# Kernel tuning notes

Measured on AMD Instinct MI355X. Metric: run time of the kernel, lower is better.

## Reference

```python
import jax, jax.numpy as jnp
import numpy as np

# dims (must match init_kwargs / input_specs)
B_SZ = 1024
STOCH = 1024
ACT = 32
DETER = 4096
TOKENS = 8
TOKEN_DIM = DETER // TOKENS          # 512
EXPAND = 2
HIDDEN = EXPAND * TOKEN_DIM          # 1024
NHEADS = 8
HEADDIM = HIDDEN // NHEADS           # 128
DSTATE = 64
K = 4                                # conv kernel
LAYERS = 2
CONV_DIM = HIDDEN + 2 * DSTATE       # 1152
IN_PROJ_DIM = HIDDEN + CONV_DIM + NHEADS
EPS = 1e-4


def rmsnorm(x, w):
    return x * jax.lax.rsqrt(jnp.mean(x * x, axis=-1, keepdims=True) + EPS) * w


def silu(x):
    return x * jax.nn.sigmoid(x)


def setup_inputs() -> dict:
    key = jax.random.key(0)
    ks = jax.random.split(key, 16)

    def lin(k, shape, fan_in):
        return jax.random.normal(k, shape, jnp.float32) / np.sqrt(fan_in)

    # dt_bias init (inverse softplus of log-uniform dt in [1e-3, 1e-1])
    u = jax.random.uniform(ks[0], (LAYERS, NHEADS))
    dt = jnp.exp(u * (np.log(0.1) - np.log(0.001)) + np.log(0.001))
    dt = jnp.maximum(dt, 1e-4)
    dt_bias = dt + jnp.log(-jnp.expm1(-dt))

    return {
        "stoch": jax.random.normal(ks[1], (B_SZ, STOCH), jnp.float32),
        "deter": jax.random.normal(ks[2], (B_SZ, DETER), jnp.float32),
        "action": jax.random.normal(ks[3], (B_SZ, ACT), jnp.float32),
        "conv_state": jax.random.normal(ks[4], (LAYERS, B_SZ, CONV_DIM, K - 1), jnp.float32),
        "ssm_state": jax.random.normal(ks[5], (LAYERS, B_SZ, NHEADS, HEADDIM, DSTATE), jnp.float32),
        # input_proj: Linear(stoch+act -> token_dim) + RMSNorm + SiLU
        "in_proj_w": lin(ks[6], (TOKEN_DIM, STOCH + ACT), STOCH + ACT),
        "in_proj_b": jnp.zeros((TOKEN_DIM,), jnp.float32),
        "in_norm_w": jnp.ones((TOKEN_DIM,), jnp.float32),
        # per-block params, stacked over layers
        "blk_norm_w": jnp.ones((LAYERS, TOKEN_DIM), jnp.float32),
        "blk_in_w": lin(ks[7], (LAYERS, IN_PROJ_DIM, TOKEN_DIM), TOKEN_DIM),
        "blk_conv_w": lin(ks[8], (LAYERS, CONV_DIM, K), K),
        "blk_conv_b": jnp.zeros((LAYERS, CONV_DIM), jnp.float32),
        "blk_A_log": jnp.log(jax.random.uniform(ks[9], (LAYERS, NHEADS), minval=1.0, maxval=16.0)),
        "blk_D": jnp.ones((LAYERS, NHEADS), jnp.float32),
        "blk_dt_bias": dt_bias.astype(jnp.float32),
        "blk_post_norm_w": jnp.ones((LAYERS, HIDDEN), jnp.float32),
        "blk_out_w": lin(ks[10], (LAYERS, TOKEN_DIM, HIDDEN), HIDDEN),
        "blk_out_b": jnp.zeros((LAYERS, TOKEN_DIM), jnp.float32),
        "out_norm_w": jnp.ones((TOKEN_DIM,), jnp.float32),
    }


def reference(stoch, deter, action, conv_state, ssm_state,
              in_proj_w, in_proj_b, in_norm_w,
              blk_norm_w, blk_in_w, blk_conv_w, blk_conv_b,
              blk_A_log, blk_D, blk_dt_bias, blk_post_norm_w,
              blk_out_w, blk_out_b, out_norm_w):
    b = action.shape[0]
    # action normalization with detached denominator
    action = action / jax.lax.stop_gradient(jnp.maximum(jnp.abs(action), 1.0))
    inp = jnp.concatenate([stoch.reshape(b, -1), action], axis=-1)
    tok = silu(rmsnorm(inp @ in_proj_w.T + in_proj_b, in_norm_w))  # (B, token_dim)

    def block_step(x, layer):
        nw, iw, cw, cb, alog, dskip, dtb, pw, ow, ob, cs, ss = layer
        h = rmsnorm(x, nw)
        proj = h @ iw.T  # (B, hidden + conv_dim + nheads)
        z = proj[:, :HIDDEN]
        xBC = proj[:, HIDDEN:HIDDEN + CONV_DIM]
        dt_raw = proj[:, HIDDEN + CONV_DIM:]
        # depthwise causal conv on xBC with persistent state
        seq = jnp.concatenate([cs, xBC[:, :, None]], axis=-1)  # (B, conv_dim, K)
        conv = silu(jnp.einsum('ck,bck->bc', cw, seq) + cb)
        new_cs = seq[:, :, 1:]
        x_post = conv[:, :HIDDEN]
        Bp = conv[:, HIDDEN:HIDDEN + DSTATE]
        Cp = conv[:, HIDDEN + DSTATE:]
        xh = x_post.reshape(b, NHEADS, HEADDIM)
        # SSD single-step recurrence
        dt = jax.nn.softplus(dt_raw + dtb)           # (B, H)
        dA = jnp.exp(dt * (-jnp.exp(alog)))          # (B, H)
        dBx = jnp.einsum('bh,bn,bhp->bhpn', dt, Bp, xh)
        new_ss = ss * dA[:, :, None, None] + dBx     # (B, H, P, N)
        y = jnp.einsum('bhpn,bn->bhp', new_ss, Cp) + dskip[None, :, None] * xh
        gated = rmsnorm(y.reshape(b, HIDDEN) * silu(z), pw)
        out = gated @ ow.T + ob
        return x + out, (new_cs, new_ss)

    layers = (blk_norm_w, blk_in_w, blk_conv_w, blk_conv_b, blk_A_log, blk_D,
              blk_dt_bias, blk_post_norm_w, blk_out_w, blk_out_b,
              conv_state, ssm_state)
    x_final, (new_conv_state, new_ssm_state) = jax.lax.scan(block_step, tok, layers)

    x_t = rmsnorm(x_final, out_norm_w)  # (B, token_dim)
    # rolling tape of last TOKENS final-block outputs
    tape = deter.reshape(b, TOKENS, TOKEN_DIM)
    new_deter = jnp.concatenate([tape[:, 1:], x_t[:, None, :]], axis=1).reshape(b, DETER)
    return (new_deter, new_conv_state, new_ssm_state)
```

## Files before the change

### kernel.cpp

```cpp
#include <hip/hip_runtime.h>
#include <hip/hip_bf16.h>
#include <math.h>

#define B_SZ 1024
#define STOCH 1024
#define ACT 32
#define DETER 4096
#define TOKEN_DIM 512
#define HIDDEN 1024
#define NHEADS 8
#define HEADDIM 128
#define DSTATE 64
#define CONV_DIM 1152
#define IN_PROJ_DIM 2184
#define IPP2 2304
#define KIN 1088
#define EPS 0.0001f

typedef float f32x4 __attribute__((ext_vector_type(4)));
typedef __bf16 bf16x8 __attribute__((ext_vector_type(8)));
typedef __bf16 bf16x4 __attribute__((ext_vector_type(4)));

#define N0C (512 * KIN / 4)
#define N1C (2 * IPP2 * TOKEN_DIM / 4)
#define N2C (2 * TOKEN_DIM * HIDDEN / 4)
#define N3C (B_SZ * KIN / 4)
__global__ __launch_bounds__(256) void prep_all(
    const float* __restrict__ inproj, const float* __restrict__ blkin,
    const float* __restrict__ blkout,
    const float* __restrict__ stoch, const float* __restrict__ action,
    __bf16* __restrict__ w0, __bf16* __restrict__ w1, __bf16* __restrict__ w2,
    __bf16* __restrict__ inp)
{
    int i = blockIdx.x * 256 + threadIdx.x;
    bf16x4 o = { (__bf16)0.f, (__bf16)0.f, (__bf16)0.f, (__bf16)0.f };
    if (i < N0C) {
        int idx = i * 4;
        int rr = idx / KIN, cc = idx % KIN;
        if (cc < STOCH + ACT) {
            float4 v = *(const float4*)(inproj + (size_t)rr * (STOCH + ACT) + cc);
            o = bf16x4{ (__bf16)v.x, (__bf16)v.y, (__bf16)v.z, (__bf16)v.w };
        }
        ((bf16x4*)w0)[i] = o;
    } else if (i < N0C + N1C) {
        int j = i - N0C;
        int idx = j * 4;
        int li  = idx / (IPP2 * TOKEN_DIM);
        int rem = idx % (IPP2 * TOKEN_DIM);
        int rr  = rem / TOKEN_DIM, cc = rem % TOKEN_DIM;
        if (rr < IN_PROJ_DIM) {
            float4 v = *(const float4*)(blkin + ((size_t)li * IN_PROJ_DIM + rr) * TOKEN_DIM + cc);
            o = bf16x4{ (__bf16)v.x, (__bf16)v.y, (__bf16)v.z, (__bf16)v.w };
        }
        ((bf16x4*)w1)[j] = o;
    } else if (i < N0C + N1C + N2C) {
        int j = i - N0C - N1C;
        float4 v = ((const float4*)blkout)[j];
        o = bf16x4{ (__bf16)v.x, (__bf16)v.y, (__bf16)v.z, (__bf16)v.w };
        ((bf16x4*)w2)[j] = o;
    } else if (i < N0C + N1C + N2C + N3C) {
        int j = i - N0C - N1C - N2C;
        int idx = j * 4;
        int b = idx / KIN, c = idx % KIN;
        if (c < STOCH) {
            float4 v = *(const float4*)(stoch + (size_t)b * STOCH + c);
            o = bf16x4{ (__bf16)v.x, (__bf16)v.y, (__bf16)v.z, (__bf16)v.w };
        } else if (c < STOCH + ACT) {
            float4 v = *(const float4*)(action + (size_t)b * ACT + (c - STOCH));
            float4 m;
            m.x = fabsf(v.x) > 1.f ? fabsf(v.x) : 1.f;
            m.y = fabsf(v.y) > 1.f ? fabsf(v.y) : 1.f;
            m.z = fabsf(v.z) > 1.f ? fabsf(v.z) : 1.f;
            m.w = fabsf(v.w) > 1.f ? fabsf(v.w) : 1.f;
            o = bf16x4{ (__bf16)(v.x / m.x), (__bf16)(v.y / m.y),
                        (__bf16)(v.z / m.z), (__bf16)(v.w / m.w) };
        }
        ((bf16x4*)inp)[j] = o;
    }
}

template<bool SPLIT, typename OutT>
__global__ __launch_bounds__(256) void gemm_v2(
    const __bf16* __restrict__ A,
    const __bf16* __restrict__ W,
    const float* __restrict__ bias,
    OutT* __restrict__ C,
    int M, int N, int K, int chunk_steps)
{
    __shared__ __bf16 As[128 * 64];
    __shared__ __bf16 Ws[64 * 64];
    const int tid = threadIdx.x;
    const int bn = blockIdx.x * 64;
    const int bm = blockIdx.y * 128;
    const int nsteps = K >> 6;
    int s_begin = 0, s_end = nsteps;
    OutT* Cout = C;
    if (SPLIT) {
        int z = blockIdx.z;
        s_begin = z * chunk_steps;
        int se = s_begin + chunk_steps;
        s_end = se < nsteps ? se : nsteps;
        Cout = C + (size_t)z * M * N;
    }

    const int wid = tid >> 6;
    const int lane = tid & 63;
    const int wr = wid * 32;
    const int r = lane & 15;
    const int kb = (lane >> 4) * 16;

    const int row0 = tid >> 3;
    const int colb = (tid & 7) * 16;
    const int wof = row0 * 128 + (colb ^ ((row0 & 7) << 4));
    char* Asb = (char*)As;
    char* Wsb = (char*)Ws;

    const __bf16* gA = A + (size_t)(bm + row0) * K + (s_begin << 6) + (colb >> 1);
    const __bf16* gW = W + (size_t)(bn + row0) * K + (s_begin << 6) + (colb >> 1);
    const size_t aK32 = (size_t)32 * K;

    const int ar0 = wr + r;
    const int ar1 = wr + 16 + r;
    const int aswz = (ar0 & 7) << 4;
    const int bswz = (r & 7) << 4;

    f32x4 acc[2][4] = {};
    bf16x8 va0 = *(const bf16x8*)(gA);
    bf16x8 va1 = *(const bf16x8*)(gA + aK32);
    bf16x8 va2 = *(const bf16x8*)(gA + 2 * aK32);
    bf16x8 va3 = *(const bf16x8*)(gA + 3 * aK32);
    bf16x8 vw0 = *(const bf16x8*)(gW);
    bf16x8 vw1 = *(const bf16x8*)(gW + aK32);

    for (int s = s_begin; s < s_end; ++s) {
        __syncthreads();
        *(bf16x8*)(Asb + wof) = va0;
        *(bf16x8*)(Asb + wof + 32 * 128) = va1;
        *(bf16x8*)(Asb + wof + 64 * 128) = va2;
        *(bf16x8*)(Asb + wof + 96 * 128) = va3;
        *(bf16x8*)(Wsb + wof) = vw0;
        *(bf16x8*)(Wsb + wof + 32 * 128) = vw1;
        __syncthreads();
        if (s + 1 < s_end) {
            const int ko = (s + 1 - s_begin) << 6;
            va0 = *(const bf16x8*)(gA + ko);
            va1 = *(const bf16x8*)(gA + aK32 + ko);
            va2 = *(const bf16x8*)(gA + 2 * aK32 + ko);
            va3 = *(const bf16x8*)(gA + 3 * aK32 + ko);
            vw0 = *(const bf16x8*)(gW + ko);
            vw1 = *(const bf16x8*)(gW + aK32 + ko);
        }
        #pragma unroll
        for (int ks = 0; ks < 2; ++ks) {
            const int cb = ks * 64 + kb;
            bf16x8 a0 = *(const bf16x8*)(Asb + ar0 * 128 + (cb ^ aswz));
            bf16x8 a1 = *(const bf16x8*)(Asb + ar1 * 128 + (cb ^ aswz));
            bf16x8 b0 = *(const bf16x8*)(Wsb + r * 128 + (cb ^ bswz));
            bf16x8 b1 = *(const bf16x8*)(Wsb + (r + 16) * 128 + (cb ^ bswz));
            bf16x8 b2 = *(const bf16x8*)(Wsb + (r + 32) * 128 + (cb ^ bswz));
            bf16x8 b3 = *(const bf16x8*)(Wsb + (r + 48) * 128 + (cb ^ bswz));
            acc[0][0] = __builtin_amdgcn_mfma_f32_16x16x32_bf16(a0, b0, acc[0][0], 0, 0, 0);
            acc[0][1] = __builtin_amdgcn_mfma_f32_16x16x32_bf16(a0, b1, acc[0][1], 0, 0, 0);
            acc[0][2] = __builtin_amdgcn_mfma_f32_16x16x32_bf16(a0, b2, acc[0][2], 0, 0, 0);
            acc[0][3] = __builtin_amdgcn_mfma_f32_16x16x32_bf16(a0, b3, acc[0][3], 0, 0, 0);
            acc[1][0] = __builtin_amdgcn_mfma_f32_16x16x32_bf16(a1, b0, acc[1][0], 0, 0, 0);
            acc[1][1] = __builtin_amdgcn_mfma_f32_16x16x32_bf16(a1, b1, acc[1][1], 0, 0, 0);
            acc[1][2] = __builtin_amdgcn_mfma_f32_16x16x32_bf16(a1, b2, acc[1][2], 0, 0, 0);
            acc[1][3] = __builtin_amdgcn_mfma_f32_16x16x32_bf16(a1, b3, acc[1][3], 0, 0, 0);
        }
    }

    const int cr = (lane >> 4) * 4;
    const int cc = lane & 15;
    #pragma unroll
    for (int mi = 0; mi < 2; mi++) {
        #pragma unroll
        for (int ni = 0; ni < 4; ni++) {
            int n = bn + ni * 16 + cc;
            #pragma unroll
            for (int j = 0; j < 4; j++) {
                int m = bm + wr + mi * 16 + cr + j;
                float v = acc[mi][ni][j];
                if (!SPLIT && bias) v += bias[n];
                Cout[(size_t)m * N + n] = (OutT)v;
            }
        }
    }
}

__device__ __forceinline__ float block_sum(float v, float* red, int t) {
    #pragma unroll
    for (int off = 32; off >= 1; off >>= 1) v += __shfl_xor(v, off);
    if ((t & 63) == 0) red[t >> 6] = v;
    __syncthreads();
    float tot = red[0] + red[1] + red[2] + red[3];
    __syncthreads();
    return tot;
}

__global__ __launch_bounds__(256) void reduce_in_kernel(
    const float* __restrict__ P,
    const float* __restrict__ bias,
    const float* __restrict__ inw,
    const float* __restrict__ nw,
    float* __restrict__ X, __bf16* __restrict__ Hb)
{
    __shared__ float red[4];
    int b = blockIdx.x, t = threadIdx.x;
    const size_t stride = (size_t)B_SZ * TOKEN_DIM;
    float h[2];
    float ss = 0.f;
    #pragma unroll
    for (int i = 0; i < 2; i++) {
        int c = t + i * 256;
        size_t o = (size_t)b * TOKEN_DIM + c;
        float v = P[o] + P[o + stride] + P[o + 2 * stride] + P[o + 3 * stride] + bias[c];
        h[i] = v;
        ss += v * v;
    }
    float tot = block_sum(ss, red, t);
    float sc = rsqrtf(tot / (float)TOKEN_DIM + EPS);
    float ss2 = 0.f;
    #pragma unroll
    for (int i = 0; i < 2; i++) {
        int c = t + i * 256;
        float v = h[i] * sc * inw[c];
        v = v / (1.f + expf(-v));
        h[i] = v;
        X[(size_t)b * TOKEN_DIM + c] = v;
        ss2 += v * v;
    }
    float tot2 = block_sum(ss2, red, t);
    float sc2 = rsqrtf(tot2 / (float)TOKEN_DIM + EPS);
    #pragma unroll
    for (int i = 0; i < 2; i++) {
        int c = t + i * 256;
        Hb[(size_t)b * TOKEN_DIM + c] = (__bf16)(h[i] * sc2 * nw[c]);
    }
}

template<int MODE>
__global__ __launch_bounds__(256) void reduce_out_kernel(
    const float* __restrict__ P,
    const float* __restrict__ ob,
    const float* __restrict__ Xin,
    const float* __restrict__ w,
    float* __restrict__ X,
    __bf16* __restrict__ Hb,
    const float* __restrict__ deter,
    float* __restrict__ out)
{
    __shared__ float red[4];
    int b = blockIdx.x, t = threadIdx.x;
    const size_t stride = (size_t)B_SZ * TOKEN_DIM;
    float h[2];
    float ss = 0.f;
    #pragma unroll
    for (int i = 0; i < 2; i++) {
        int c = t + i * 256;
        size_t o = (size_t)b * TOKEN_DIM + c;
        float v = Xin[o] + P[o] + P[o + stride] + P[o + 2 * stride] + P[o + 3 * stride] + ob[c];
        h[i] = v;
        ss += v * v;
    }
    float tot = block_sum(ss, red, t);
    float sc = rsqrtf(tot / (float)TOKEN_DIM + EPS);
    if (MODE == 0) {
        #pragma unroll
        for (int i = 0; i < 2; i++) {
            int c = t + i * 256;
            size_t o = (size_t)b * TOKEN_DIM + c;
            X[o] = h[i];
            Hb[o] = (__bf16)(h[i] * sc * w[c]);
        }
    } else {
        #pragma unroll
        for (int i = 0; i < 2; i++) {
            int c = t + i * 256;
            out[(size_t)b * DETER + 3584 + c] = h[i] * sc * w[c];
        }
        const float4* src = (const float4*)(deter + (size_t)b * DETER + TOKEN_DIM);
        float4* dst = (float4*)(out + (size_t)b * DETER);
        #pragma unroll
        for (int j = 0; j < 4; ++j) {
            int idx = t + j * 256;
            if (idx < 896) dst[idx] = src[idx];
        }
    }
}

__global__ __launch_bounds__(256, 4) void conv_ssm_gate_kernel(
    const float* __restrict__ cs,
    const __bf16* __restrict__ proj,
    const float* __restrict__ cw,
    const float* __restrict__ cb,
    const float* __restrict__ dtb,
    const float* __restrict__ alog,
    const float* __restrict__ Dv,
    const float* __restrict__ pw,
    const float* __restrict__ ss,
    float* __restrict__ new_cs,
    float* __restrict__ new_ss,
    __bf16* __restrict__ Gb)
{
    __shared__ float convs[CONV_DIM];
    __shared__ float yrow[HIDDEN];
    __shared__ float dts[NHEADS], dAs[NHEADS], dvs[NHEADS];
    __shared__ float red[4];

    int b = blockIdx.x, t = threadIdx.x;
    const __bf16* prow = proj + (size_t)b * IPP2;

    const int p0 = t >> 4;
    const int nq = (t & 15) * 4;
    const float* basep = ss + (size_t)b * NHEADS * HEADDIM * DSTATE;
    float* baseo = new_ss + (size_t)b * NHEADS * HEADDIM * DSTATE;

    f32x4 cur[8], nxt[8];
    #pragma unroll
    for (int it = 0; it < 8; ++it) {
        int p = it * 16 + p0;
        cur[it] = __builtin_nontemporal_load((const f32x4*)(basep + (size_t)p * DSTATE + nq));
    }

    if (t < NHEADS) {
        float dtr = (float)prow[HIDDEN + CONV_DIM + t] + dtb[t];
        float dt = dtr > 20.f ? dtr : log1pf(expf(dtr));
        dts[t] = dt;
        dAs[t] = expf(dt * -expf(alog[t]));
        dvs[t] = Dv[t];
    }
    for (int c = t; c < CONV_DIM; c += 256) {
        const float* s = cs + ((size_t)b * CONV_DIM + c) * 3;
        float s0 = s[0], s1 = s[1], s2 = s[2];
        float xbc = (float)prow[HIDDEN + c];
        float4 wv = *(const float4*)(cw + c * 4);
        float v = wv.x * s0 + wv.y * s1 + wv.z * s2 + wv.w * xbc + cb[c];
        v = v / (1.f + expf(-v));
        convs[c] = v;
        float* nc = new_cs + ((size_t)b * CONV_DIM + c) * 3;
        nc[0] = s1; nc[1] = s2; nc[2] = xbc;
    }
    __syncthreads();

    const f32x4 Bv = *(const f32x4*)&convs[HIDDEN + nq];
    const f32x4 Cv = *(const f32x4*)&convs[HIDDEN + DSTATE + nq];

    #pragma unroll
    for (int h = 0; h < NHEADS; ++h) {
        if (h + 1 < NHEADS) {
            #pragma unroll
            for (int it = 0; it < 8; ++it) {
                int p = it * 16 + p0;
                nxt[it] = __builtin_nontemporal_load(
                    (const f32x4*)(basep + (size_t)((h + 1) * HEADDIM + p) * DSTATE + nq));
            }
        }
        const float dt = dts[h], dA = dAs[h], Dk = dvs[h];
        float* op = baseo + (size_t)h * HEADDIM * DSTATE;
        #pragma unroll
        for (int it = 0; it < 8; ++it) {
            int p = it * 16 + p0;
            float xp = convs[h * HEADDIM + p];
            float dtx = dt * xp;
            f32x4 o = cur[it] * dA + dtx * Bv;
            __builtin_nontemporal_store(o, (f32x4*)(op + (size_t)p * DSTATE + nq));
            f32x4 a4 = o * Cv;
            float acc = (a4[0] + a4[1]) + (a4[2] + a4[3]);
            acc += __shfl_xor(acc, 1);
            acc += __shfl_xor(acc, 2);
            acc += __shfl_xor(acc, 4);
            acc += __shfl_xor(acc, 8);
            if ((t & 15) == 0) yrow[h * HEADDIM + p] = acc + Dk * xp;
        }
        if (h + 1 < NHEADS) {
            #pragma unroll
            for (int it = 0; it < 8; ++it) cur[it] = nxt[it];
        }
    }
    __syncthreads();

    float vv[4];
    float ssum = 0.f;
    #pragma unroll
    for (int i = 0; i < 4; i++) {
        int j = t + i * 256;
        float z = (float)prow[j];
        float val = yrow[j] * (z / (1.f + expf(-z)));
        vv[i] = val;
        ssum += val * val;
    }
    float tot = block_sum(ssum, red, t);
    float sc = rsqrtf(tot / (float)HIDDEN + EPS);
    #pragma unroll
    for (int i = 0; i < 4; i++) {
        int j = t + i * 256;
        Gb[(size_t)b * HIDDEN + j] = (__bf16)(vv[i] * sc * pw[j]);
    }
}

extern "C" void kernel_launch(void* const* d_in, const int* in_sizes, int n_in,
                              void* d_out, int out_size, void* d_ws, size_t ws_size,
                              hipStream_t stream) {
    const float* stoch      = (const float*)d_in[0];
    const float* deter      = (const float*)d_in[1];
    const float* action     = (const float*)d_in[2];
    const float* conv_state = (const float*)d_in[3];
    const float* ssm_state  = (const float*)d_in[4];
    const float* in_proj_w  = (const float*)d_in[5];
    const float* in_proj_b  = (const float*)d_in[6];
    const float* in_norm_w  = (const float*)d_in[7];
    const float* blk_norm_w = (const float*)d_in[8];
    const float* blk_in_w   = (const float*)d_in[9];
    const float* blk_conv_w = (const float*)d_in[10];
    const float* blk_conv_b = (const float*)d_in[11];
    const float* blk_A_log  = (const float*)d_in[12];
    const float* blk_D      = (const float*)d_in[13];
    const float* blk_dt_bias= (const float*)d_in[14];
    const float* blk_post_norm_w = (const float*)d_in[15];
    const float* blk_out_w  = (const float*)d_in[16];
    const float* blk_out_b  = (const float*)d_in[17];
    const float* out_norm_w = (const float*)d_in[18];

    float* out_deter = (float*)d_out;
    float* out_cs    = out_deter + (size_t)B_SZ * DETER;
    float* out_ss    = out_cs + (size_t)2 * B_SZ * CONV_DIM * 3;

    char* ws = (char*)d_ws;
    __bf16* Wb_inproj = (__bf16*)ws;  ws += (size_t)TOKEN_DIM * KIN * 2;
    __bf16* Wb_blkin  = (__bf16*)ws;  ws += (size_t)2 * IPP2 * TOKEN_DIM * 2;
    __bf16* Wb_blkout = (__bf16*)ws;  ws += (size_t)2 * TOKEN_DIM * HIDDEN * 2;
    float*  X         = (float*)ws;   ws += (size_t)B_SZ * TOKEN_DIM * 4;
    __bf16* Hb        = (__bf16*)ws;  ws += (size_t)B_SZ * TOKEN_DIM * 2;
    __bf16* PROJ      = (__bf16*)ws;  ws += (size_t)B_SZ * IPP2 * 2;
    __bf16* Gb        = (__bf16*)ws;  ws += (size_t)B_SZ * HIDDEN * 2;
    float*  PART      = (float*)ws;   ws += (size_t)4 * B_SZ * TOKEN_DIM * 4;
    __bf16* INPb = PROJ;

    {
        int total = N0C + N1C + N2C + N3C;
        prep_all<<<(total + 255) / 256, 256, 0, stream>>>(
            in_proj_w, blk_in_w, blk_out_w, stoch, action,
            Wb_inproj, Wb_blkin, Wb_blkout, INPb);
    }
    {
        dim3 grid(TOKEN_DIM / 64, B_SZ / 128, 4);
        gemm_v2<true, float><<<grid, 256, 0, stream>>>(INPb, Wb_inproj, nullptr, PART,
                                                       B_SZ, TOKEN_DIM, KIN, 5);
        reduce_in_kernel<<<B_SZ, 256, 0, stream>>>(PART, in_proj_b, in_norm_w,
                                                   blk_norm_w, X, Hb);
    }

    for (int l = 0; l < 2; ++l) {
        const __bf16* iw = Wb_blkin + (size_t)l * IPP2 * TOKEN_DIM;
        const float* cw  = blk_conv_w + (size_t)l * CONV_DIM * 4;
        const float* cbv = blk_conv_b + (size_t)l * CONV_DIM;
        const float* alog= blk_A_log + (size_t)l * NHEADS;
        const float* Dvv = blk_D + (size_t)l * NHEADS;
        const float* dtb = blk_dt_bias + (size_t)l * NHEADS;
        const float* pw  = blk_post_norm_w + (size_t)l * HIDDEN;
        const __bf16* ow = Wb_blkout + (size_t)l * TOKEN_DIM * HIDDEN;
        const float* ob  = blk_out_b + (size_t)l * TOKEN_DIM;
        const float* cs_in = conv_state + (size_t)l * B_SZ * CONV_DIM * 3;
        const float* ss_in = ssm_state + (size_t)l * B_SZ * NHEADS * HEADDIM * DSTATE;
        float* cs_out = out_cs + (size_t)l * B_SZ * CONV_DIM * 3;
        float* ss_out = out_ss + (size_t)l * B_SZ * NHEADS * HEADDIM * DSTATE;

        {
            dim3 grid(IPP2 / 64, B_SZ / 128);
            gemm_v2<false, __bf16><<<grid, 256, 0, stream>>>(Hb, iw, nullptr, PROJ,
                                                             B_SZ, IPP2, TOKEN_DIM, 0);
        }
        conv_ssm_gate_kernel<<<B_SZ, 256, 0, stream>>>(
            cs_in, PROJ, cw, cbv, dtb, alog, Dvv, pw, ss_in, cs_out, ss_out, Gb);
        {
            dim3 grid(TOKEN_DIM / 64, B_SZ / 128, 4);
            gemm_v2<true, float><<<grid, 256, 0, stream>>>(Gb, ow, nullptr, PART,
                                                           B_SZ, TOKEN_DIM, HIDDEN, 4);
        }
        if (l == 0) {
            reduce_out_kernel<0><<<B_SZ, 256, 0, stream>>>(
                PART, ob, X, blk_norm_w + TOKEN_DIM, X, Hb, nullptr, nullptr);
        } else {
            reduce_out_kernel<1><<<B_SZ, 256, 0, stream>>>(
                PART, ob, X, out_norm_w, nullptr, nullptr, deter, out_deter);
        }
    }
}
```

Before: 279.2 us.

## Convert fp32 block weights to bf16 inside GEMM loads and halve split-K

Drops the separate pass that converted the block in/out projection weights to bf16. The GEMM now reads fp32 weights directly and converts them while staging into shared memory, with row masking in place of the padded weight buffer. Split-K for the input and output projections drops from 4 chunks to 2, so the reduce kernels sum fewer partials. The cost is more global bytes per weight load inside the GEMM and fewer workgroups for the split GEMMs.

```diff
diff --git a/kernel.cpp b/kernel.cpp
--- a/kernel.cpp
+++ b/kernel.cpp
@@ -21,16 +21,19 @@
 typedef __bf16 bf16x8 __attribute__((ext_vector_type(8)));
 typedef __bf16 bf16x4 __attribute__((ext_vector_type(4)));
 
+__device__ __forceinline__ bf16x8 cvt8(float4 a, float4 b) {
+    bf16x8 r;
+    r[0] = (__bf16)a.x; r[1] = (__bf16)a.y; r[2] = (__bf16)a.z; r[3] = (__bf16)a.w;
+    r[4] = (__bf16)b.x; r[5] = (__bf16)b.y; r[6] = (__bf16)b.z; r[7] = (__bf16)b.w;
+    return r;
+}
+
 #define N0C (512 * KIN / 4)
-#define N1C (2 * IPP2 * TOKEN_DIM / 4)
-#define N2C (2 * TOKEN_DIM * HIDDEN / 4)
 #define N3C (B_SZ * KIN / 4)
-__global__ __launch_bounds__(256) void prep_all(
-    const float* __restrict__ inproj, const float* __restrict__ blkin,
-    const float* __restrict__ blkout,
+__global__ __launch_bounds__(256) void prep_small(
+    const float* __restrict__ inproj,
     const float* __restrict__ stoch, const float* __restrict__ action,
-    __bf16* __restrict__ w0, __bf16* __restrict__ w1, __bf16* __restrict__ w2,
-    __bf16* __restrict__ inp)
+    __bf16* __restrict__ w0, __bf16* __restrict__ inp)
 {
     int i = blockIdx.x * 256 + threadIdx.x;
     bf16x4 o = { (__bf16)0.f, (__bf16)0.f, (__bf16)0.f, (__bf16)0.f };
@@ -42,24 +45,8 @@
             o = bf16x4{ (__bf16)v.x, (__bf16)v.y, (__bf16)v.z, (__bf16)v.w };
         }
         ((bf16x4*)w0)[i] = o;
-    } else if (i < N0C + N1C) {
+    } else if (i < N0C + N3C) {
         int j = i - N0C;
-        int idx = j * 4;
-        int li  = idx / (IPP2 * TOKEN_DIM);
-        int rem = idx % (IPP2 * TOKEN_DIM);
-        int rr  = rem / TOKEN_DIM, cc = rem % TOKEN_DIM;
-        if (rr < IN_PROJ_DIM) {
-            float4 v = *(const float4*)(blkin + ((size_t)li * IN_PROJ_DIM + rr) * TOKEN_DIM + cc);
-            o = bf16x4{ (__bf16)v.x, (__bf16)v.y, (__bf16)v.z, (__bf16)v.w };
-        }
-        ((bf16x4*)w1)[j] = o;
-    } else if (i < N0C + N1C + N2C) {
-        int j = i - N0C - N1C;
-        float4 v = ((const float4*)blkout)[j];
-        o = bf16x4{ (__bf16)v.x, (__bf16)v.y, (__bf16)v.z, (__bf16)v.w };
-        ((bf16x4*)w2)[j] = o;
-    } else if (i < N0C + N1C + N2C + N3C) {
-        int j = i - N0C - N1C - N2C;
         int idx = j * 4;
         int b = idx / KIN, c = idx % KIN;
         if (c < STOCH) {
@@ -79,13 +66,13 @@
     }
 }
 
-template<bool SPLIT, typename OutT>
+template<bool SPLIT, bool WF32, typename OutT>
 __global__ __launch_bounds__(256) void gemm_v2(
     const __bf16* __restrict__ A,
-    const __bf16* __restrict__ W,
+    const void* __restrict__ Wp,
     const float* __restrict__ bias,
     OutT* __restrict__ C,
-    int M, int N, int K, int chunk_steps)
+    int M, int N, int Nreal, int K, int chunk_steps)
 {
     __shared__ __bf16 As[128 * 64];
     __shared__ __bf16 Ws[64 * 64];
@@ -111,12 +98,12 @@
 
     const int row0 = tid >> 3;
     const int colb = (tid & 7) * 16;
+    const int e0   = colb >> 1;
     const int wof = row0 * 128 + (colb ^ ((row0 & 7) << 4));
     char* Asb = (char*)As;
     char* Wsb = (char*)Ws;
 
-    const __bf16* gA = A + (size_t)(bm + row0) * K + (s_begin << 6) + (colb >> 1);
-    const __bf16* gW = W + (size_t)(bn + row0) * K + (s_begin << 6) + (colb >> 1);
+    const __bf16* gA = A + (size_t)(bm + row0) * K + (s_begin << 6) + e0;
     const size_t aK32 = (size_t)32 * K;
 
     const int ar0 = wr + r;
@@ -129,8 +116,25 @@
     bf16x8 va1 = *(const bf16x8*)(gA + aK32);
     bf16x8 va2 = *(const bf16x8*)(gA + 2 * aK32);
     bf16x8 va3 = *(const bf16x8*)(gA + 3 * aK32);
-    bf16x8 vw0 = *(const bf16x8*)(gW);
-    bf16x8 vw1 = *(const bf16x8*)(gW + aK32);
+
+    const bool v0 = (bn + row0) < Nreal;
+    const bool v1 = (bn + row0 + 32) < Nreal;
+    bf16x8 vw0 = {}, vw1 = {};
+    const __bf16* gW = nullptr;
+    const float*  gWf0 = nullptr, *gWf1 = nullptr;
+    if (WF32) {
+        gWf0 = (const float*)Wp + (size_t)(bn + row0) * K + (s_begin << 6) + e0;
+        gWf1 = gWf0 + (size_t)32 * K;
+        float4 wa0{}, wb0{}, wa1{}, wb1{};
+        if (v0) { wa0 = *(const float4*)gWf0; wb0 = *(const float4*)(gWf0 + 4); }
+        if (v1) { wa1 = *(const float4*)gWf1; wb1 = *(const float4*)(gWf1 + 4); }
+        vw0 = cvt8(wa0, wb0);
+        vw1 = cvt8(wa1, wb1);
+    } else {
+        gW = (const __bf16*)Wp + (size_t)(bn + row0) * K + (s_begin << 6) + e0;
+        if (v0) vw0 = *(const bf16x8*)(gW);
+        if (v1) vw1 = *(const bf16x8*)(gW + aK32);
+    }
 
     for (int s = s_begin; s < s_end; ++s) {
         __syncthreads();
@@ -147,8 +151,16 @@
             va1 = *(const bf16x8*)(gA + aK32 + ko);
             va2 = *(const bf16x8*)(gA + 2 * aK32 + ko);
             va3 = *(const bf16x8*)(gA + 3 * aK32 + ko);
-            vw0 = *(const bf16x8*)(gW + ko);
-            vw1 = *(const bf16x8*)(gW + aK32 + ko);
+            if (WF32) {
+                float4 wa0{}, wb0{}, wa1{}, wb1{};
+                if (v0) { wa0 = *(const float4*)(gWf0 + ko); wb0 = *(const float4*)(gWf0 + ko + 4); }
+                if (v1) { wa1 = *(const float4*)(gWf1 + ko); wb1 = *(const float4*)(gWf1 + ko + 4); }
+                vw0 = cvt8(wa0, wb0);
+                vw1 = cvt8(wa1, wb1);
+            } else {
+                if (v0) vw0 = *(const bf16x8*)(gW + ko);
+                if (v1) vw1 = *(const bf16x8*)(gW + aK32 + ko);
+            }
         }
         #pragma unroll
         for (int ks = 0; ks < 2; ++ks) {
@@ -214,7 +226,7 @@
     for (int i = 0; i < 2; i++) {
         int c = t + i * 256;
         size_t o = (size_t)b * TOKEN_DIM + c;
-        float v = P[o] + P[o + stride] + P[o + 2 * stride] + P[o + 3 * stride] + bias[c];
+        float v = P[o] + P[o + stride] + bias[c];
         h[i] = v;
         ss += v * v;
     }
@@ -259,7 +271,7 @@
     for (int i = 0; i < 2; i++) {
         int c = t + i * 256;
         size_t o = (size_t)b * TOKEN_DIM + c;
-        float v = Xin[o] + P[o] + P[o + stride] + P[o + 2 * stride] + P[o + 3 * stride] + ob[c];
+        float v = Xin[o] + P[o] + P[o + stride] + ob[c];
         h[i] = v;
         ss += v * v;
     }
@@ -428,38 +440,35 @@
 
     char* ws = (char*)d_ws;
     __bf16* Wb_inproj = (__bf16*)ws;  ws += (size_t)TOKEN_DIM * KIN * 2;
-    __bf16* Wb_blkin  = (__bf16*)ws;  ws += (size_t)2 * IPP2 * TOKEN_DIM * 2;
-    __bf16* Wb_blkout = (__bf16*)ws;  ws += (size_t)2 * TOKEN_DIM * HIDDEN * 2;
     float*  X         = (float*)ws;   ws += (size_t)B_SZ * TOKEN_DIM * 4;
     __bf16* Hb        = (__bf16*)ws;  ws += (size_t)B_SZ * TOKEN_DIM * 2;
     __bf16* PROJ      = (__bf16*)ws;  ws += (size_t)B_SZ * IPP2 * 2;
     __bf16* Gb        = (__bf16*)ws;  ws += (size_t)B_SZ * HIDDEN * 2;
-    float*  PART      = (float*)ws;   ws += (size_t)4 * B_SZ * TOKEN_DIM * 4;
+    float*  PART      = (float*)ws;   ws += (size_t)2 * B_SZ * TOKEN_DIM * 4;
     __bf16* INPb = PROJ;
 
     {
-        int total = N0C + N1C + N2C + N3C;
-        prep_all<<<(total + 255) / 256, 256, 0, stream>>>(
-            in_proj_w, blk_in_w, blk_out_w, stoch, action,
-            Wb_inproj, Wb_blkin, Wb_blkout, INPb);
+        int total = N0C + N3C;
+        prep_small<<<(total + 255) / 256, 256, 0, stream>>>(
+            in_proj_w, stoch, action, Wb_inproj, INPb);
     }
     {
-        dim3 grid(TOKEN_DIM / 64, B_SZ / 128, 4);
-        gemm_v2<true, float><<<grid, 256, 0, stream>>>(INPb, Wb_inproj, nullptr, PART,
-                                                       B_SZ, TOKEN_DIM, KIN, 5);
+        dim3 grid(TOKEN_DIM / 64, B_SZ / 128, 2);
+        gemm_v2<true, false, float><<<grid, 256, 0, stream>>>(
+            INPb, Wb_inproj, nullptr, PART, B_SZ, TOKEN_DIM, TOKEN_DIM, KIN, 9);
         reduce_in_kernel<<<B_SZ, 256, 0, stream>>>(PART, in_proj_b, in_norm_w,
                                                    blk_norm_w, X, Hb);
     }
 
     for (int l = 0; l < 2; ++l) {
-        const __bf16* iw = Wb_blkin + (size_t)l * IPP2 * TOKEN_DIM;
+        const float* iw  = blk_in_w + (size_t)l * IN_PROJ_DIM * TOKEN_DIM;
         const float* cw  = blk_conv_w + (size_t)l * CONV_DIM * 4;
         const float* cbv = blk_conv_b + (size_t)l * CONV_DIM;
         const float* alog= blk_A_log + (size_t)l * NHEADS;
         const float* Dvv = blk_D + (size_t)l * NHEADS;
         const float* dtb = blk_dt_bias + (size_t)l * NHEADS;
         const float* pw  = blk_post_norm_w + (size_t)l * HIDDEN;
-        const __bf16* ow = Wb_blkout + (size_t)l * TOKEN_DIM * HIDDEN;
+        const float* ow  = blk_out_w + (size_t)l * TOKEN_DIM * HIDDEN;
         const float* ob  = blk_out_b + (size_t)l * TOKEN_DIM;
         const float* cs_in = conv_state + (size_t)l * B_SZ * CONV_DIM * 3;
         const float* ss_in = ssm_state + (size_t)l * B_SZ * NHEADS * HEADDIM * DSTATE;
@@ -468,15 +477,15 @@
 
         {
             dim3 grid(IPP2 / 64, B_SZ / 128);
-            gemm_v2<false, __bf16><<<grid, 256, 0, stream>>>(Hb, iw, nullptr, PROJ,
-                                                             B_SZ, IPP2, TOKEN_DIM, 0);
+            gemm_v2<false, true, __bf16><<<grid, 256, 0, stream>>>(
+                Hb, iw, nullptr, PROJ, B_SZ, IPP2, IN_PROJ_DIM, TOKEN_DIM, 0);
         }
         conv_ssm_gate_kernel<<<B_SZ, 256, 0, stream>>>(
             cs_in, PROJ, cw, cbv, dtb, alog, Dvv, pw, ss_in, cs_out, ss_out, Gb);
         {
-            dim3 grid(TOKEN_DIM / 64, B_SZ / 128, 4);
-            gemm_v2<true, float><<<grid, 256, 0, stream>>>(Gb, ow, nullptr, PART,
-                                                           B_SZ, TOKEN_DIM, HIDDEN, 4);
+            dim3 grid(TOKEN_DIM / 64, B_SZ / 128, 2);
+            gemm_v2<true, true, float><<<grid, 256, 0, stream>>>(
+                Gb, ow, nullptr, PART, B_SZ, TOKEN_DIM, TOKEN_DIM, HIDDEN, 8);
         }
         if (l == 0) {
             reduce_out_kernel<0><<<B_SZ, 256, 0, stream>>>(
```

Measured after the change: 297.8 us. 1.07x slower.
